# Kernel tuning notes

Measured on AMD Instinct MI355X. Metric: run time of the kernel, lower is better.

## Reference

```python
import jax, jax.numpy as jnp
import numpy as np

N = 50000      # B*N nodes
K = 32         # top-k in-degree
E = N * K      # edges
IN_DIM = 128
EMB_DIM = 128
OUT_DIM = 128
HEADS = 4
D_HEAD = OUT_DIM // HEADS


def setup_inputs() -> dict:
    key = jax.random.key(0)
    ks = jax.random.split(key, 8)
    x = jax.random.normal(ks[0], (N, IN_DIM), dtype=jnp.float32)
    emb = jax.random.normal(ks[1], (N, EMB_DIM), dtype=jnp.float32)
    # top-k graph: each node i has exactly K in-neighbors (dst covers all nodes)
    dst = jnp.repeat(jnp.arange(N, dtype=jnp.int32), K)
    src = jax.random.randint(ks[2], (E,), 0, N, dtype=jnp.int32)
    edge_index = jnp.stack([src, dst], axis=0)
    # learned params (stored as (in, out); math-equivalent to torch Linear)
    W_q = jax.random.normal(ks[3], (EMB_DIM, OUT_DIM), dtype=jnp.float32) / np.sqrt(EMB_DIM)
    W_k = jax.random.normal(ks[4], (EMB_DIM, OUT_DIM), dtype=jnp.float32) / np.sqrt(EMB_DIM)
    W_v = jax.random.normal(ks[5], (IN_DIM + EMB_DIM, OUT_DIM), dtype=jnp.float32) / np.sqrt(IN_DIM + EMB_DIM)
    attn_vec = jax.random.normal(ks[6], (HEADS, 2 * D_HEAD), dtype=jnp.float32) / np.sqrt(2 * D_HEAD)
    ln_gamma = jnp.ones((OUT_DIM,), dtype=jnp.float32)
    ln_beta = jnp.zeros((OUT_DIM,), dtype=jnp.float32)
    return {"x": x, "emb": emb, "edge_index": edge_index, "W_q": W_q, "W_k": W_k,
            "W_v": W_v, "attn_vec": attn_vec, "ln_gamma": ln_gamma, "ln_beta": ln_beta}


def reference(x, emb, edge_index, W_q, W_k, W_v, attn_vec, ln_gamma, ln_beta):
    src, dst = edge_index[0], edge_index[1]
    BN = x.shape[0]
    H, D = HEADS, D_HEAD
    Q = (emb @ W_q).reshape(BN, H, D)
    K_ = (emb @ W_k).reshape(BN, H, D)
    # a^T [q_dst || k_src] = (a_q . q)_dst + (a_k . k)_src  (standard GAT split)
    a_q, a_k = attn_vec[:, :D], attn_vec[:, D:]
    sq = jnp.einsum('nhd,hd->nh', Q, a_q)   # (BN, H)
    sk = jnp.einsum('nhd,hd->nh', K_, a_k)  # (BN, H)
    e = sq[dst] + sk[src]                   # (E, H)
    e = jnp.where(e > 0, e, 0.2 * e)        # LeakyReLU(0.2)
    # segment softmax over incoming edges of each dst node
    e_max = jax.ops.segment_max(e, dst, num_segments=BN)
    e_exp = jnp.exp(e - e_max[dst])
    e_sum = jax.ops.segment_sum(e_exp, dst, num_segments=BN)
    alpha = e_exp / (e_sum[dst] + 1e-8)     # (E, H); dropout is identity at eval
    V = (jnp.concatenate([x, emb], axis=-1) @ W_v).reshape(BN, H, D)
    weighted = alpha[..., None] * V[src]    # (E, H, D)
    z = jax.ops.segment_sum(weighted, dst, num_segments=BN).reshape(BN, H * D)
    z = jax.nn.elu(z)
    mu = jnp.mean(z, axis=-1, keepdims=True)
    var = jnp.var(z, axis=-1, keepdims=True)
    return (z - mu) / jnp.sqrt(var + 1e-5) * ln_gamma + ln_beta
```

## Files before the change

### kernel.cpp

```cpp
#include <hip/hip_runtime.h>

#define NN 50000
#define KE 32
#define PAD_N 50048

using f32x4  = __attribute__((ext_vector_type(4))) float;
using bf16x8 = __attribute__((ext_vector_type(8))) short;

__device__ __forceinline__ ushort f2bf(float f) {
    union { float f; unsigned u; } c; c.f = f;
    unsigned u = c.u;
    u += 0x7fffu + ((u >> 16) & 1u);
    return (ushort)(u >> 16);
}
__device__ __forceinline__ ushort f2h(float f) {
    union { _Float16 h; ushort u; } c; c.h = (_Float16)f; return c.u;
}
__device__ __forceinline__ float h2f(ushort u) {
    union { ushort u; _Float16 h; } c; c.u = u; return (float)c.h;
}

__global__ __launch_bounds__(256) void prep_kernel(const float* __restrict__ Wq,
        const float* __restrict__ Wk, const float* __restrict__ av,
        const float* __restrict__ Wv, ushort* __restrict__ Ub,
        ushort* __restrict__ Bt) {
    const int g = blockIdx.x * 256 + threadIdx.x;
    if (blockIdx.x < 2) {
        const int h = g >> 7, i = g & 127;
        float su = 0.f, sv = 0.f;
#pragma unroll
        for (int d = 0; d < 32; ++d) {
            su += Wq[i * 128 + h * 32 + d] * av[h * 64 + d];
            sv += Wk[i * 128 + h * 32 + d] * av[h * 64 + 32 + d];
        }
        Ub[h * 128 + i] = f2bf(su);
        Ub[(4 + h) * 128 + i] = f2bf(sv);
        Ub[1024 + g * 2] = 0;
        Ub[1024 + g * 2 + 1] = 0;
    } else {
        const int idx = g - 512;
        const int k = idx >> 7, n = idx & 127;
        Bt[n * 256 + k] = f2bf(Wv[idx]);
    }
}

__global__ __launch_bounds__(256) void vproj_mfma(const float* __restrict__ x,
        const float* __restrict__ emb, const ushort* __restrict__ Bt,
        const ushort* __restrict__ Ub, float* __restrict__ sq,
        float* __restrict__ sk, ushort* __restrict__ Vp) {
    __shared__ short As[64 * 264];
    const int t = threadIdx.x;
    const int rbase = blockIdx.x * 64;
    const int wv = t >> 6;
    const int lane = t & 63;
    const int lo = lane & 15;
    const int quad = lane >> 4;
    const int c0 = wv * 32;

#pragma unroll
    for (int it = 0; it < 16; ++it) {
        const int li = it * 256 + t;
        const int row = li >> 6;
        const int c4 = li & 63;
        int rg = rbase + row; if (rg >= NN) rg = NN - 1;
        const float* sp = (c4 < 32) ? (x + (long)rg * 128 + c4 * 4)
                                    : (emb + (long)rg * 128 + (c4 - 32) * 4);
        float4 a = *(const float4*)sp;
        ushort4 b = make_ushort4(f2bf(a.x), f2bf(a.y), f2bf(a.z), f2bf(a.w));
        *(ushort4*)&As[row * 264 + c4 * 4] = b;
    }
    bf16x8 bt0[8], bt1[8];
#pragma unroll
    for (int ks = 0; ks < 8; ++ks) {
        const int kb = ks * 32 + quad * 8;
        bt0[ks] = *(const bf16x8*)(Bt + (c0 + lo) * 256 + kb);
        bt1[ks] = *(const bf16x8*)(Bt + (c0 + 16 + lo) * 256 + kb);
    }
    __syncthreads();

    f32x4 acc[4][2] = {};
#pragma unroll
    for (int ks = 0; ks < 8; ++ks) {
        const int kb = ks * 32 + quad * 8;
#pragma unroll
        for (int rt = 0; rt < 4; ++rt) {
            bf16x8 af = *(const bf16x8*)&As[(rt * 16 + lo) * 264 + kb];
            acc[rt][0] = __builtin_amdgcn_mfma_f32_16x16x32_bf16(af, bt0[ks], acc[rt][0], 0, 0, 0);
            acc[rt][1] = __builtin_amdgcn_mfma_f32_16x16x32_bf16(af, bt1[ks], acc[rt][1], 0, 0, 0);
        }
    }

    f32x4 sacc = {};
#pragma unroll
    for (int ks = 0; ks < 4; ++ks) {
        const int kk = ks * 32 + quad * 8;
        bf16x8 saf = *(const bf16x8*)&As[(wv * 16 + lo) * 264 + 128 + kk];
        bf16x8 sbf = *(const bf16x8*)(Ub + lo * 128 + kk);
        sacc = __builtin_amdgcn_mfma_f32_16x16x32_bf16(saf, sbf, sacc, 0, 0, 0);
    }
    if (lo < 8) {
#pragma unroll
        for (int r = 0; r < 4; ++r) {
            const int row = rbase + wv * 16 + quad * 4 + r;
            if (row < NN) {
                if (lo < 4) sq[(long)row * 4 + lo] = sacc[r];
                else        sk[(long)row * 4 + lo - 4] = sacc[r];
            }
        }
    }

    __syncthreads();
#pragma unroll
    for (int rt = 0; rt < 4; ++rt)
#pragma unroll
        for (int ct = 0; ct < 2; ++ct)
#pragma unroll
            for (int r = 0; r < 4; ++r)
                As[(rt * 16 + quad * 4 + r) * 132 + c0 + ct * 16 + lo] =
                    (short)f2bf(acc[rt][ct][r]);
    __syncthreads();
#pragma unroll
    for (int i = 0; i < 4; ++i) {
        const int idx = i * 256 + t;
        const int row = idx >> 4;
        const int seg = idx & 15;
        const int grow = rbase + row;
        const int plane = seg >> 2;
        const int pc = (seg & 3) * 8;
        if (grow < NN)
            *(bf16x8*)(Vp + (long)plane * PAD_N * 32 + (long)grow * 32 + pc) =
                *(const bf16x8*)&As[row * 132 + seg * 8];
    }
}

__global__ __launch_bounds__(256) void alpha_kernel(const int* __restrict__ src,
        const float* __restrict__ sq, const float* __restrict__ sk,
        ushort* __restrict__ alpha) {
    const int t = threadIdx.x;
    const int e = t & 31;
    const int n = blockIdx.x * 8 + (t >> 5);
    const int s = src[(long)n * KE + e];
    float4 sk4 = *(const float4*)(sk + (long)s * 4);
    float4 sq4 = *(const float4*)(sq + (long)n * 4);
    float ev[4] = { sq4.x + sk4.x, sq4.y + sk4.y, sq4.z + sk4.z, sq4.w + sk4.w };
#pragma unroll
    for (int h = 0; h < 4; ++h) ev[h] = ev[h] > 0.f ? ev[h] : 0.2f * ev[h];
    float m[4] = { ev[0], ev[1], ev[2], ev[3] };
#pragma unroll
    for (int off = 16; off > 0; off >>= 1) {
#pragma unroll
        for (int h = 0; h < 4; ++h) m[h] = fmaxf(m[h], __shfl_xor(m[h], off));
    }
    float ex[4], sum[4];
#pragma unroll
    for (int h = 0; h < 4; ++h) { ex[h] = __expf(ev[h] - m[h]); sum[h] = ex[h]; }
#pragma unroll
    for (int off = 16; off > 0; off >>= 1) {
#pragma unroll
        for (int h = 0; h < 4; ++h) sum[h] += __shfl_xor(sum[h], off);
    }
#pragma unroll
    for (int h = 0; h < 4; ++h)
        alpha[(long)n * 128 + h * 32 + e] = f2h(ex[h] / (sum[h] + 1e-8f));
}

__global__ __launch_bounds__(256) void gather_kernel(const int* __restrict__ src,
        const ushort* __restrict__ alpha, const ushort* __restrict__ Vp,
        float* __restrict__ z) {
    __shared__ int   s_src[32 * 33];
    __shared__ float s_al [32 * 33];
    const int b = blockIdx.x;
    const int head = (b & 7) >> 1;
    const int chunk = (b >> 3) * 2 + (b & 1);
    const int nbase = chunk * 32;
    const int t = threadIdx.x;

#pragma unroll
    for (int i = 0; i < 4; ++i) {
        const int idx = i * 256 + t;
        const int n = idx >> 5, e = idx & 31;
        const int nn = nbase + n;
        s_src[n * 33 + e] = (nn < NN) ? src[(long)nn * KE + e] : 0;
        const ushort a = (nn < NN) ? alpha[(long)nn * 128 + head * 32 + e] : 0;
        s_al[n * 33 + e] = h2f(a);
    }
    __syncthreads();

    const int slot = t >> 3;
    const int l = t & 7;
    const int node = nbase + slot;
    const ushort* plane = Vp + (long)head * PAD_N * 32;
    float z0 = 0.f, z1 = 0.f, z2 = 0.f, z3 = 0.f;
#pragma unroll 8
    for (int e = 0; e < 32; ++e) {
        const int sidx = s_src[slot * 33 + e];
        const float a = s_al[slot * 33 + e];
        uint2 p = *(const uint2*)(plane + (long)sidx * 32 + l * 4);
        union { unsigned u; float f; } e0, o0, e1, o1;
        e0.u = p.x << 16; o0.u = p.x & 0xffff0000u;
        e1.u = p.y << 16; o1.u = p.y & 0xffff0000u;
        z0 += a * e0.f; z1 += a * o0.f; z2 += a * e1.f; z3 += a * o1.f;
    }
    if (node < NN)
        *(float4*)(z + (long)node * 128 + head * 32 + l * 4) =
            make_float4(z0, z1, z2, z3);
}

__global__ __launch_bounds__(256) void lnorm_kernel(float* __restrict__ z,
        const float* __restrict__ gamma, const float* __restrict__ beta) {
    const int w = threadIdx.x >> 6;
    const int lane = threadIdx.x & 63;
    const int n = blockIdx.x * 4 + w;
    const int c0 = lane * 2;
    float2 zv = *(const float2*)(z + (long)n * 128 + c0);
    float zx = zv.x, zy = zv.y;
    zx = zx > 0.f ? zx : __expf(zx) - 1.f;
    zy = zy > 0.f ? zy : __expf(zy) - 1.f;
    float s1 = zx + zy;
    float s2 = zx * zx + zy * zy;
#pragma unroll
    for (int off = 32; off > 0; off >>= 1) {
        s1 += __shfl_xor(s1, off);
        s2 += __shfl_xor(s2, off);
    }
    const float mu = s1 * (1.f / 128.f);
    const float var = s2 * (1.f / 128.f) - mu * mu;
    const float rstd = rsqrtf(var + 1e-5f);
    float2 g = *(const float2*)(gamma + c0);
    float2 b = *(const float2*)(beta + c0);
    float2 o;
    o.x = (zx - mu) * rstd * g.x + b.x;
    o.y = (zy - mu) * rstd * g.y + b.y;
    *(float2*)(z + (long)n * 128 + c0) = o;
}

extern "C" void kernel_launch(void* const* d_in, const int* in_sizes, int n_in,
                              void* d_out, int out_size, void* d_ws, size_t ws_size,
                              hipStream_t stream) {
    const float* x     = (const float*)d_in[0];
    const float* emb   = (const float*)d_in[1];
    const int*   edge  = (const int*)d_in[2];
    const float* Wq    = (const float*)d_in[3];
    const float* Wk    = (const float*)d_in[4];
    const float* Wv    = (const float*)d_in[5];
    const float* av    = (const float*)d_in[6];
    const float* gamma = (const float*)d_in[7];
    const float* beta  = (const float*)d_in[8];
    float* out = (float*)d_out;

    char* ws = (char*)d_ws;
    ushort* Ub    = (ushort*)(ws + 0);
    ushort* Bt    = (ushort*)(ws + 4096);
    float*  sq    = (float*)(ws + 69632);
    float*  sk    = (float*)(ws + 869632);
    ushort* alpha = (ushort*)(ws + 1669632);
    ushort* Vp    = (ushort*)(ws + 14469632);

    prep_kernel<<<130, 256, 0, stream>>>(Wq, Wk, av, Wv, Ub, Bt);
    vproj_mfma<<<(NN + 63) / 64, 256, 0, stream>>>(x, emb, Bt, Ub, sq, sk, Vp);
    alpha_kernel<<<NN / 8, 256, 0, stream>>>(edge, sq, sk, alpha);
    gather_kernel<<<782 * 8, 256, 0, stream>>>(edge, alpha, Vp, out);
    lnorm_kernel<<<NN / 4, 256, 0, stream>>>(out, gamma, beta);
}
```

Before: 196.1 us.

## Fuse attention softmax into gather kernel and transpose score layout

Removes the separate alpha kernel and computes the per-head segment softmax inside the gather kernel, storing alpha directly in shared memory. sq/sk are written head-major so each gather block reads a contiguous plane. The gather now handles 64 nodes per block with 16-byte vector loads per lane. This eliminates the fp16 alpha buffer round-trip and a launch, at the cost of recomputing the softmax scores per head block and more work per thread.

```diff
diff --git a/kernel.cpp b/kernel.cpp
--- a/kernel.cpp
+++ b/kernel.cpp
@@ -12,12 +12,6 @@
     unsigned u = c.u;
     u += 0x7fffu + ((u >> 16) & 1u);
     return (ushort)(u >> 16);
-}
-__device__ __forceinline__ ushort f2h(float f) {
-    union { _Float16 h; ushort u; } c; c.h = (_Float16)f; return c.u;
-}
-__device__ __forceinline__ float h2f(ushort u) {
-    union { ushort u; _Float16 h; } c; c.u = u; return (float)c.h;
 }
 
 __global__ __launch_bounds__(256) void prep_kernel(const float* __restrict__ Wq,
@@ -46,8 +40,8 @@
 
 __global__ __launch_bounds__(256) void vproj_mfma(const float* __restrict__ x,
         const float* __restrict__ emb, const ushort* __restrict__ Bt,
-        const ushort* __restrict__ Ub, float* __restrict__ sq,
-        float* __restrict__ sk, ushort* __restrict__ Vp) {
+        const ushort* __restrict__ Ub, float* __restrict__ sqT,
+        float* __restrict__ skT, ushort* __restrict__ Vp) {
     __shared__ short As[64 * 264];
     const int t = threadIdx.x;
     const int rbase = blockIdx.x * 64;
@@ -103,8 +97,8 @@
         for (int r = 0; r < 4; ++r) {
             const int row = rbase + wv * 16 + quad * 4 + r;
             if (row < NN) {
-                if (lo < 4) sq[(long)row * 4 + lo] = sacc[r];
-                else        sk[(long)row * 4 + lo - 4] = sacc[r];
+                if (lo < 4) sqT[(long)lo * NN + row] = sacc[r];
+                else        skT[(long)(lo - 4) * NN + row] = sacc[r];
             }
         }
     }
@@ -133,77 +127,68 @@
     }
 }
 
-__global__ __launch_bounds__(256) void alpha_kernel(const int* __restrict__ src,
-        const float* __restrict__ sq, const float* __restrict__ sk,
-        ushort* __restrict__ alpha) {
-    const int t = threadIdx.x;
-    const int e = t & 31;
-    const int n = blockIdx.x * 8 + (t >> 5);
-    const int s = src[(long)n * KE + e];
-    float4 sk4 = *(const float4*)(sk + (long)s * 4);
-    float4 sq4 = *(const float4*)(sq + (long)n * 4);
-    float ev[4] = { sq4.x + sk4.x, sq4.y + sk4.y, sq4.z + sk4.z, sq4.w + sk4.w };
-#pragma unroll
-    for (int h = 0; h < 4; ++h) ev[h] = ev[h] > 0.f ? ev[h] : 0.2f * ev[h];
-    float m[4] = { ev[0], ev[1], ev[2], ev[3] };
-#pragma unroll
-    for (int off = 16; off > 0; off >>= 1) {
-#pragma unroll
-        for (int h = 0; h < 4; ++h) m[h] = fmaxf(m[h], __shfl_xor(m[h], off));
-    }
-    float ex[4], sum[4];
-#pragma unroll
-    for (int h = 0; h < 4; ++h) { ex[h] = __expf(ev[h] - m[h]); sum[h] = ex[h]; }
-#pragma unroll
-    for (int off = 16; off > 0; off >>= 1) {
-#pragma unroll
-        for (int h = 0; h < 4; ++h) sum[h] += __shfl_xor(sum[h], off);
-    }
-#pragma unroll
-    for (int h = 0; h < 4; ++h)
-        alpha[(long)n * 128 + h * 32 + e] = f2h(ex[h] / (sum[h] + 1e-8f));
-}
-
 __global__ __launch_bounds__(256) void gather_kernel(const int* __restrict__ src,
-        const ushort* __restrict__ alpha, const ushort* __restrict__ Vp,
-        float* __restrict__ z) {
-    __shared__ int   s_src[32 * 33];
-    __shared__ float s_al [32 * 33];
+        const float* __restrict__ sqT, const float* __restrict__ skT,
+        const ushort* __restrict__ Vp, float* __restrict__ z) {
+    __shared__ int   s_src[64 * 33];
+    __shared__ float s_al [64 * 33];
     const int b = blockIdx.x;
     const int head = (b & 7) >> 1;
     const int chunk = (b >> 3) * 2 + (b & 1);
-    const int nbase = chunk * 32;
+    const int nbase = chunk * 64;
     const int t = threadIdx.x;
-
-#pragma unroll
-    for (int i = 0; i < 4; ++i) {
-        const int idx = i * 256 + t;
-        const int n = idx >> 5, e = idx & 31;
-        const int nn = nbase + n;
-        s_src[n * 33 + e] = (nn < NN) ? src[(long)nn * KE + e] : 0;
-        const ushort a = (nn < NN) ? alpha[(long)nn * 128 + head * 32 + e] : 0;
-        s_al[n * 33 + e] = h2f(a);
-    }
-    __syncthreads();
-
-    const int slot = t >> 3;
-    const int l = t & 7;
+    const int e = t & 31;
+
+    const float* sqh = sqT + (long)head * NN;
+    const float* skh = skT + (long)head * NN;
+#pragma unroll
+    for (int p = 0; p < 8; ++p) {
+        const int slot = p * 8 + (t >> 5);
+        const int n = nbase + slot;
+        const bool valid = n < NN;
+        const int s = valid ? src[(long)n * KE + e] : 0;
+        float ev = valid ? (sqh[n] + skh[s]) : 0.f;
+        ev = ev > 0.f ? ev : 0.2f * ev;
+        float m = ev;
+#pragma unroll
+        for (int off = 16; off > 0; off >>= 1)
+            m = fmaxf(m, __shfl_xor(m, off));
+        const float ex = __expf(ev - m);
+        float sum = ex;
+#pragma unroll
+        for (int off = 16; off > 0; off >>= 1)
+            sum += __shfl_xor(sum, off);
+        s_src[slot * 33 + e] = s;
+        s_al[slot * 33 + e] = ex / (sum + 1e-8f);
+    }
+    __syncthreads();
+
+    const int slot = t >> 2;
+    const int l = t & 3;
+    const ushort* plane = Vp + (long)head * PAD_N * 32 + l * 8;
+    float z0 = 0.f, z1 = 0.f, z2 = 0.f, z3 = 0.f;
+    float z4 = 0.f, z5 = 0.f, z6 = 0.f, z7 = 0.f;
+#pragma unroll 16
+    for (int ee = 0; ee < 32; ++ee) {
+        const int sidx = s_src[slot * 33 + ee];
+        const float a = s_al[slot * 33 + ee];
+        uint4 p = *(const uint4*)(plane + (long)sidx * 32);
+        union { unsigned u; float f; } c0e, c0o, c1e, c1o, c2e, c2o, c3e, c3o;
+        c0e.u = p.x << 16; c0o.u = p.x & 0xffff0000u;
+        c1e.u = p.y << 16; c1o.u = p.y & 0xffff0000u;
+        c2e.u = p.z << 16; c2o.u = p.z & 0xffff0000u;
+        c3e.u = p.w << 16; c3o.u = p.w & 0xffff0000u;
+        z0 += a * c0e.f; z1 += a * c0o.f;
+        z2 += a * c1e.f; z3 += a * c1o.f;
+        z4 += a * c2e.f; z5 += a * c2o.f;
+        z6 += a * c3e.f; z7 += a * c3o.f;
+    }
     const int node = nbase + slot;
-    const ushort* plane = Vp + (long)head * PAD_N * 32;
-    float z0 = 0.f, z1 = 0.f, z2 = 0.f, z3 = 0.f;
-#pragma unroll 8
-    for (int e = 0; e < 32; ++e) {
-        const int sidx = s_src[slot * 33 + e];
-        const float a = s_al[slot * 33 + e];
-        uint2 p = *(const uint2*)(plane + (long)sidx * 32 + l * 4);
-        union { unsigned u; float f; } e0, o0, e1, o1;
-        e0.u = p.x << 16; o0.u = p.x & 0xffff0000u;
-        e1.u = p.y << 16; o1.u = p.y & 0xffff0000u;
-        z0 += a * e0.f; z1 += a * o0.f; z2 += a * e1.f; z3 += a * o1.f;
-    }
-    if (node < NN)
-        *(float4*)(z + (long)node * 128 + head * 32 + l * 4) =
-            make_float4(z0, z1, z2, z3);
+    if (node < NN) {
+        float* zp = z + (long)node * 128 + head * 32 + l * 8;
+        *(float4*)(zp)     = make_float4(z0, z1, z2, z3);
+        *(float4*)(zp + 4) = make_float4(z4, z5, z6, z7);
+    }
 }
 
 __global__ __launch_bounds__(256) void lnorm_kernel(float* __restrict__ z,
@@ -249,16 +234,14 @@
     float* out = (float*)d_out;
 
     char* ws = (char*)d_ws;
-    ushort* Ub    = (ushort*)(ws + 0);
-    ushort* Bt    = (ushort*)(ws + 4096);
-    float*  sq    = (float*)(ws + 69632);
-    float*  sk    = (float*)(ws + 869632);
-    ushort* alpha = (ushort*)(ws + 1669632);
-    ushort* Vp    = (ushort*)(ws + 14469632);
+    ushort* Ub  = (ushort*)(ws + 0);
+    ushort* Bt  = (ushort*)(ws + 4096);
+    float*  sqT = (float*)(ws + 69632);
+    float*  skT = (float*)(ws + 869632);
+    ushort* Vp  = (ushort*)(ws + 1669632);
 
     prep_kernel<<<130, 256, 0, stream>>>(Wq, Wk, av, Wv, Ub, Bt);
-    vproj_mfma<<<(NN + 63) / 64, 256, 0, stream>>>(x, emb, Bt, Ub, sq, sk, Vp);
-    alpha_kernel<<<NN / 8, 256, 0, stream>>>(edge, sq, sk, alpha);
-    gather_kernel<<<782 * 8, 256, 0, stream>>>(edge, alpha, Vp, out);
+    vproj_mfma<<<(NN + 63) / 64, 256, 0, stream>>>(x, emb, Bt, Ub, sqT, skT, Vp);
+    gather_kernel<<<782 * 4, 256, 0, stream>>>(edge, sqT, skT, Vp, out);
     lnorm_kernel<<<NN / 4, 256, 0, stream>>>(out, gamma, beta);
 }
```

Result: no change. 195.7 us (-0.2%).
